# Performance work log

Hardware: AMD Instinct MI355X
Metric: run time of the kernel (lower is better)

Reference implementation:

```python
import jax, jax.numpy as jnp
import numpy as np

D_MODEL = 1024
NUM_HEADS = 16
HEAD_DIM = D_MODEL // NUM_HEADS


def setup_inputs() -> dict:
    key = jax.random.key(0)
    ks = jax.random.split(key, 9)
    B, L, D = 2, 2048, D_MODEL
    s = 1.0 / np.sqrt(D)
    return {
        "x": jax.random.normal(ks[0], (B, L, D), dtype=jnp.float32),
        "Wq": jax.random.normal(ks[1], (D, D), dtype=jnp.float32) * s,
        "bq": jax.random.normal(ks[2], (D,), dtype=jnp.float32) * 0.01,
        "Wk": jax.random.normal(ks[3], (D, D), dtype=jnp.float32) * s,
        "bk": jax.random.normal(ks[4], (D,), dtype=jnp.float32) * 0.01,
        "Wv": jax.random.normal(ks[5], (D, D), dtype=jnp.float32) * s,
        "bv": jax.random.normal(ks[6], (D,), dtype=jnp.float32) * 0.01,
        "Wo": jax.random.normal(ks[7], (D, D), dtype=jnp.float32) * s,
        "bo": jax.random.normal(ks[8], (D,), dtype=jnp.float32) * 0.01,
    }


def reference(x, Wq, bq, Wk, bk, Wv, bv, Wo, bo):
    B, L, D = x.shape
    H, hd = NUM_HEADS, HEAD_DIM
    # projections (torch Linear: x @ W^T + b)
    q = (x @ Wq.T + bq).reshape(B, L, H, hd).transpose(0, 2, 1, 3)  # [B,H,L,hd]
    k = (x @ Wk.T + bk).reshape(B, L, H, hd).transpose(0, 2, 1, 3)
    v = (x @ Wv.T + bv).reshape(B, L, H, hd).transpose(0, 2, 1, 3)
    scores = jnp.einsum("bhqd,bhkd->bhqk", q, k) / jnp.sqrt(jnp.float32(hd))
    attn = jax.nn.softmax(scores, axis=-1)
    ctx = jnp.einsum("bhqk,bhkd->bhqd", attn, v)  # [B,H,L,hd]
    ctx = ctx.transpose(0, 2, 1, 3).reshape(B, L, D)
    return ctx @ Wo.T + bo
```

## Files before the change

### kernel.cpp

```cpp
#include <hip/hip_runtime.h>
#include <hip/hip_bf16.h>
#include <stdint.h>

typedef __attribute__((ext_vector_type(8))) short short8;
typedef __attribute__((ext_vector_type(4))) float f32x4;
typedef __attribute__((ext_vector_type(16))) float f32x16;
typedef __attribute__((ext_vector_type(4))) unsigned int uint4v;
typedef __attribute__((ext_vector_type(2))) unsigned int uint2v;

#define MFMA16(a, b, c) __builtin_amdgcn_mfma_f32_16x16x32_bf16((a), (b), (c), 0, 0, 0)
#define MFMA32(a, b, c) __builtin_amdgcn_mfma_f32_32x32x16_bf16((a), (b), (c), 0, 0, 0)

#define GLDS16(ldsptr, gptr)                                                                     \
    __builtin_amdgcn_global_load_lds(                                                            \
        (const __attribute__((address_space(1))) unsigned int*)(gptr),                           \
        (__attribute__((address_space(3))) unsigned int*)(ldsptr), 16, 0, 0)

#define WAITCNT(n) asm volatile("s_waitcnt vmcnt(" #n ")" ::: "memory")

__device__ __forceinline__ unsigned short f2bf(float f) {
    union { float f; unsigned u; } v; v.f = f;
    return (unsigned short)((v.u + 0x7FFFu + ((v.u >> 16) & 1u)) >> 16);
}

__device__ __forceinline__ unsigned cvt_pk_bf16(float lo, float hi) {
    unsigned r;
    asm("v_cvt_pk_bf16_f32 %0, %1, %2" : "=v"(r) : "v"(lo), "v"(hi));
    return r;
}

__global__ void cvt_all(const float* __restrict__ x,
                        const float* __restrict__ wq, const float* __restrict__ wk,
                        const float* __restrict__ wv, const float* __restrict__ wo,
                        unsigned short* __restrict__ xb,
                        unsigned short* __restrict__ wqb, unsigned short* __restrict__ wkb,
                        unsigned short* __restrict__ wvb, unsigned short* __restrict__ wob) {
    int bid = blockIdx.x;
    const float* s; unsigned short* d; int off;
    if (bid < 4096) {
        s = x; d = xb; off = bid;
    } else {
        int w = (bid - 4096) >> 10;
        off = (bid - 4096) & 1023;
        switch (w) {
            case 0: s = wq; d = wqb; break;
            case 1: s = wk; d = wkb; break;
            case 2: s = wv; d = wvb; break;
            default: s = wo; d = wob; break;
        }
    }
    int i = off * 256 + threadIdx.x;
    float4 v = reinterpret_cast<const float4*>(s)[i];
    ushort4 o;
    o.x = f2bf(v.x); o.y = f2bf(v.y); o.z = f2bf(v.z); o.w = f2bf(v.w);
    reinterpret_cast<ushort4*>(d)[i] = o;
}

__device__ __forceinline__ void gemm_core_mfma(
    const unsigned short* __restrict__ A, const unsigned short* __restrict__ W,
    unsigned short* sl, int m0, int n0, f32x4 (&acc)[4][4])
{
    const int tid = threadIdx.x;
    const int lane = tid & 63, wid = tid >> 6;
    const int l15 = lane & 15, grp = lane >> 4;
    const int wm = (wid >> 1) * 64, wn = (wid & 1) * 64;
    const int rs_ = tid >> 3, c8 = tid & 7;

    auto stage = [&](int buf, int kt) {
        unsigned short* As = &sl[buf * 16384];
        unsigned short* Bs = &sl[buf * 16384 + 8192];
#pragma unroll
        for (int q = 0; q < 4; ++q) {
            int r = q * 32 + rs_;
            int sc = (c8 ^ (r & 7)) << 3;
            GLDS16(&As[(q * 256 + tid) * 8], &A[(size_t)(m0 + r) * 1024 + kt + sc]);
        }
#pragma unroll
        for (int q = 0; q < 4; ++q) {
            int r = q * 32 + rs_;
            int sc = (c8 ^ (r & 7)) << 3;
            GLDS16(&Bs[(q * 256 + tid) * 8], &W[(size_t)(n0 + r) * 1024 + kt + sc]);
        }
    };

    stage(0, 0);
    for (int t = 0; t < 16; ++t) {
        if (t < 15) {
            stage((t + 1) & 1, (t + 1) * 64);
            WAITCNT(8);
        } else {
            WAITCNT(0);
        }
        __builtin_amdgcn_s_barrier();
        const unsigned short* As = &sl[(t & 1) * 16384];
        const unsigned short* Bs = &sl[(t & 1) * 16384 + 8192];
#pragma unroll
        for (int ks = 0; ks < 2; ++ks) {
            short8 a[4], b[4];
#pragma unroll
            for (int i = 0; i < 4; ++i) {
                int row = wm + i * 16 + l15;
                a[i] = *reinterpret_cast<const short8*>(
                    &As[row * 64 + ((ks * 32 + grp * 8) ^ ((row & 7) << 3))]);
            }
#pragma unroll
            for (int j = 0; j < 4; ++j) {
                int row = wn + j * 16 + l15;
                b[j] = *reinterpret_cast<const short8*>(
                    &Bs[row * 64 + ((ks * 32 + grp * 8) ^ ((row & 7) << 3))]);
            }
#pragma unroll
            for (int i = 0; i < 4; ++i)
#pragma unroll
                for (int j = 0; j < 4; ++j)
                    acc[i][j] = MFMA16(a[i], b[j], acc[i][j]);
        }
        if (t < 15) __builtin_amdgcn_s_barrier();
    }
}

__global__ __launch_bounds__(256, 2) void gemm_qkv(
    const unsigned short* __restrict__ A,
    const unsigned short* __restrict__ W0, const unsigned short* __restrict__ W1,
    const unsigned short* __restrict__ W2,
    const float* __restrict__ b0, const float* __restrict__ b1, const float* __restrict__ b2,
    unsigned short* __restrict__ o0, unsigned short* __restrict__ o1,
    unsigned short* __restrict__ vt_out)
{
    __shared__ __attribute__((aligned(16))) unsigned short sl[32768];

    int id = blockIdx.x + (blockIdx.y << 3) + (blockIdx.z << 8);
    int lg = (id & 7) * 96 + (id >> 3);
    const int bx = lg & 7, by = (lg >> 3) & 31, bz = lg >> 8;

    const unsigned short* W; const float* bias; float oscale;
    if (bz == 0)      { W = W0; bias = b0; oscale = 0.18033688f; }
    else if (bz == 1) { W = W1; bias = b1; oscale = 1.0f; }
    else              { W = W2; bias = b2; oscale = 1.0f; }

    const f32x4 fz = {0.f, 0.f, 0.f, 0.f};
    f32x4 acc[4][4];
#pragma unroll
    for (int i = 0; i < 4; ++i)
#pragma unroll
        for (int j = 0; j < 4; ++j) acc[i][j] = fz;

    const int m0 = by * 128, n0 = bx * 128;
    gemm_core_mfma(A, W, sl, m0, n0, acc);

    const int tid = threadIdx.x, lane = tid & 63, wid = tid >> 6;
    const int l15 = lane & 15, grp = lane >> 4;
    const int wm = (wid >> 1) * 64, wn = (wid & 1) * 64;
    const int bb = m0 >> 11;

    if (bz < 2) {
        unsigned short* out = (bz == 0) ? o0 : o1;
#pragma unroll
        for (int j = 0; j < 4; ++j) {
            int ncol = n0 + wn + j * 16 + l15;
            float bv_ = bias[ncol];
            int h = ncol >> 6, d = ncol & 63;
#pragma unroll
            for (int i = 0; i < 4; ++i)
#pragma unroll
                for (int r = 0; r < 4; ++r) {
                    int mrow = m0 + wm + i * 16 + grp * 4 + r;
                    int ll = mrow & 2047;
                    out[(((size_t)(bb * 16 + h)) * 2048 + ll) * 64 + d] =
                        f2bf((acc[i][j][r] + bv_) * oscale);
                }
        }
    } else {
        __syncthreads();
#pragma unroll
        for (int j = 0; j < 4; ++j) {
            float bv_ = bias[n0 + wn + j * 16 + l15];
#pragma unroll
            for (int i = 0; i < 4; ++i)
#pragma unroll
                for (int r = 0; r < 4; ++r) {
                    int c = wn + j * 16 + l15;
                    int rr = wm + i * 16 + grp * 4 + r;
                    sl[c * 136 + rr] = f2bf(acc[i][j][r] + bv_);
                }
        }
        __syncthreads();
        const int llb = m0 & 2047;
#pragma unroll 4
        for (int it = 0; it < 32; ++it) {
            int c = wid * 32 + it;
            unsigned v = *reinterpret_cast<const unsigned*>(&sl[c * 136 + lane * 2]);
            int ncol = n0 + c;
            size_t row = ((size_t)(bb * 16 + (ncol >> 6))) * 64 + (ncol & 63);
            *reinterpret_cast<unsigned*>(&vt_out[row * 2048 + llb + lane * 2]) = v;
        }
    }
}

__global__ __launch_bounds__(256, 2) void gemm_out(
    const unsigned short* __restrict__ A, const unsigned short* __restrict__ W,
    const float* __restrict__ bias, float* __restrict__ out)
{
    __shared__ __attribute__((aligned(16))) unsigned short sl[32768];

    int id = blockIdx.x + (blockIdx.y << 3);
    int lg = (id & 7) * 32 + (id >> 3);
    const int bx = lg & 7, by = lg >> 3;

    const f32x4 fz = {0.f, 0.f, 0.f, 0.f};
    f32x4 acc[4][4];
#pragma unroll
    for (int i = 0; i < 4; ++i)
#pragma unroll
        for (int j = 0; j < 4; ++j) acc[i][j] = fz;

    const int m0 = by * 128, n0 = bx * 128;
    gemm_core_mfma(A, W, sl, m0, n0, acc);

    const int tid = threadIdx.x, lane = tid & 63, wid = tid >> 6;
    const int l15 = lane & 15, grp = lane >> 4;
    const int wm = (wid >> 1) * 64, wn = (wid & 1) * 64;
#pragma unroll
    for (int j = 0; j < 4; ++j) {
        int ncol = n0 + wn + j * 16 + l15;
        float bv_ = bias[ncol];
#pragma unroll
        for (int i = 0; i < 4; ++i)
#pragma unroll
            for (int r = 0; r < 4; ++r) {
                int mrow = m0 + wm + i * 16 + grp * 4 + r;
                out[(size_t)mrow * 1024 + ncol] = acc[i][j][r] + bv_;
            }
    }
}

__global__ __launch_bounds__(512, 2) void attn_kernel(
    const unsigned short* __restrict__ Q,
    const unsigned short* __restrict__ Kg,
    const unsigned short* __restrict__ VTg,
    unsigned short* __restrict__ CTX)
{
    __shared__ __attribute__((aligned(16))) unsigned short k_s[4][4096];
    __shared__ __attribute__((aligned(16))) unsigned short vt_s[4][4096];

    const int tid = threadIdx.x, lane = tid & 63, wid = tid >> 6;
    const int l31 = lane & 31, h = lane >> 5;

    int id = blockIdx.x + (blockIdx.y << 3);
    int lg = ((id & 7) << 5) + (id >> 3);
    const int qt = lg & 7, bh = lg >> 3;

    const int rs_ = tid >> 3, c8 = tid & 7;
    const size_t kvbase = (size_t)bh * 2048 * 64;
    const size_t qbase = kvbase + (size_t)qt * 256 * 64;
    const int scv = (c8 ^ (rs_ & 7)) << 3;

    auto stageKV = [&](int t) {
        int b = t & 3;
        GLDS16(&k_s[b][tid * 8], &Kg[kvbase + (size_t)(t * 64 + rs_) * 64 + scv]);
        GLDS16(&vt_s[b][tid * 8], &VTg[kvbase + (size_t)rs_ * 2048 + t * 64 + scv]);
    };

    short8 aq[4];
    {
        const unsigned short* qp = &Q[qbase + (size_t)(wid * 32 + l31) * 64 + h * 8];
#pragma unroll
        for (int kq = 0; kq < 4; ++kq)
            aq[kq] = *reinterpret_cast<const short8*>(qp + kq * 16);
    }
    stageKV(0);
    stageKV(1);

    short8 ones;
#pragma unroll
    for (int i = 0; i < 8; ++i) ones[i] = (short)0x3F80;

    f32x16 acc[2], acc_l;
#pragma unroll
    for (int i = 0; i < 16; ++i) { acc[0][i] = 0.f; acc[1][i] = 0.f; acc_l[i] = 0.f; }

#pragma unroll 4
    for (int t = 0; t < 32; ++t) {
        if (t < 30) {
            stageKV(t + 2);
            WAITCNT(4);
        } else if (t == 30) {
            WAITCNT(2);
        } else {
            WAITCNT(0);
        }
        __builtin_amdgcn_s_barrier();
        const unsigned short* kcur = k_s[t & 3];
        const unsigned short* vcur = vt_s[t & 3];

        f32x16 st[2];
#pragma unroll
        for (int i = 0; i < 16; ++i) { st[0][i] = 0.f; st[1][i] = 0.f; }
#pragma unroll
        for (int kb = 0; kb < 2; ++kb)
#pragma unroll
            for (int kq = 0; kq < 4; ++kq) {
                int row = kb * 32 + l31;
                short8 ak = *reinterpret_cast<const short8*>(
                    &kcur[row * 64 + ((kq * 16 + h * 8) ^ ((row & 7) << 3))]);
                st[kb] = MFMA32(ak, aq[kq], st[kb]);
            }

        unsigned pk[2][4][2];
#pragma unroll
        for (int kb = 0; kb < 2; ++kb)
#pragma unroll
            for (int g = 0; g < 4; ++g)
#pragma unroll
                for (int p = 0; p < 2; ++p)
                    pk[kb][g][p] = cvt_pk_bf16(
                        __builtin_amdgcn_exp2f(st[kb][4 * g + 2 * p]),
                        __builtin_amdgcn_exp2f(st[kb][4 * g + 2 * p + 1]));

        union { uint4v u; short8 s; } ap[4];
#pragma unroll
        for (int kb = 0; kb < 2; ++kb)
#pragma unroll
            for (int j = 0; j < 2; ++j) {
                uint2v s0 = __builtin_amdgcn_permlane32_swap(
                    pk[kb][2 * j][0], pk[kb][2 * j + 1][0], false, false);
                uint2v s1 = __builtin_amdgcn_permlane32_swap(
                    pk[kb][2 * j][1], pk[kb][2 * j + 1][1], false, false);
                ap[2 * kb + j].u = (uint4v){s0[0], s1[0], s0[1], s1[1]};
            }

        __builtin_amdgcn_s_setprio(1);
#pragma unroll
        for (int kk = 0; kk < 4; ++kk) {
            acc_l = MFMA32(ap[kk].s, ones, acc_l);
#pragma unroll
            for (int db = 0; db < 2; ++db) {
                int row = db * 32 + l31;
                short8 bv = *reinterpret_cast<const short8*>(
                    &vcur[row * 64 + ((kk * 16 + h * 8) ^ ((row & 7) << 3))]);
                acc[db] = MFMA32(ap[kk].s, bv, acc[db]);
            }
        }
        __builtin_amdgcn_s_setprio(0);
    }

    const int b = bh >> 4, hh = bh & 15;
#pragma unroll
    for (int r = 0; r < 16; ++r) {
        int q_local = (r & 3) + 8 * (r >> 2) + 4 * h;
        int qrow = qt * 256 + wid * 32 + q_local;
        float inv = 1.0f / acc_l[r];
#pragma unroll
        for (int db = 0; db < 2; ++db)
            CTX[((size_t)(b * 2048 + qrow)) * 1024 + hh * 64 + db * 32 + l31] =
                f2bf(acc[db][r] * inv);
    }
}

extern "C" void kernel_launch(void* const* d_in, const int* in_sizes, int n_in,
                              void* d_out, int out_size, void* d_ws, size_t ws_size,
                              hipStream_t stream) {
    const float* x  = (const float*)d_in[0];
    const float* Wq = (const float*)d_in[1];
    const float* bq = (const float*)d_in[2];
    const float* Wk = (const float*)d_in[3];
    const float* bk = (const float*)d_in[4];
    const float* Wv = (const float*)d_in[5];
    const float* bv = (const float*)d_in[6];
    const float* Wo = (const float*)d_in[7];
    const float* bo = (const float*)d_in[8];
    float* out = (float*)d_out;

    char* ws = (char*)d_ws;
    unsigned short* xb  = (unsigned short*)(ws + ((size_t)0));
    unsigned short* wqb = (unsigned short*)(ws + ((size_t)8  << 20));
    unsigned short* wkb = (unsigned short*)(ws + ((size_t)10 << 20));
    unsigned short* wvb = (unsigned short*)(ws + ((size_t)12 << 20));
    unsigned short* wob = (unsigned short*)(ws + ((size_t)14 << 20));
    unsigned short* qb  = (unsigned short*)(ws + ((size_t)16 << 20));
    unsigned short* kb  = (unsigned short*)(ws + ((size_t)24 << 20));
    unsigned short* vt  = (unsigned short*)(ws + ((size_t)32 << 20));
    unsigned short* ctx = (unsigned short*)(ws + ((size_t)0));

    cvt_all<<<8192, 256, 0, stream>>>(x, Wq, Wk, Wv, Wo, xb, wqb, wkb, wvb, wob);

    gemm_qkv<<<dim3(8, 32, 3), 256, 0, stream>>>(xb, wqb, wkb, wvb, bq, bk, bv, qb, kb, vt);
    attn_kernel<<<dim3(8, 32), 512, 0, stream>>>(qb, kb, vt, ctx);
    gemm_out<<<dim3(8, 32), 256, 0, stream>>>(ctx, wob, bo, out);
}
```

Before: 96.75 us.

## Split attention KV tiles across wave pairs and reduce partials through LDS

Each attention block now covers 128 query rows instead of 256, using 512 blocks instead of 256. Within a block, two wave groups each handle half of every 64-key tile for the same 32 query rows. Their partial context and row-sum accumulators are combined through shared memory at the end, and launch bounds ask for 4 blocks per CU. This raises parallelism and occupancy to hide latency, at the cost of twice the K/V tile loads per query, extra barriers, an LDS reduction, and register pressure from the higher occupancy target.

New measurement: 101.0 us. 4.4% more time.

```diff
diff --git a/kernel.cpp b/kernel.cpp
--- a/kernel.cpp
+++ b/kernel.cpp
@@ -234,7 +234,7 @@
     }
 }
 
-__global__ __launch_bounds__(512, 2) void attn_kernel(
+__global__ __launch_bounds__(512, 4) void attn_kernel(
     const unsigned short* __restrict__ Q,
     const unsigned short* __restrict__ Kg,
     const unsigned short* __restrict__ VTg,
@@ -245,14 +245,15 @@
 
     const int tid = threadIdx.x, lane = tid & 63, wid = tid >> 6;
     const int l31 = lane & 31, h = lane >> 5;
-
-    int id = blockIdx.x + (blockIdx.y << 3);
-    int lg = ((id & 7) << 5) + (id >> 3);
-    const int qt = lg & 7, bh = lg >> 3;
+    const int qg = wid & 3, kh = wid >> 2;
+
+    int id = blockIdx.x + (blockIdx.y << 4);
+    int lg = ((id & 7) << 6) + (id >> 3);
+    const int qt = lg & 15, bh = lg >> 4;
 
     const int rs_ = tid >> 3, c8 = tid & 7;
     const size_t kvbase = (size_t)bh * 2048 * 64;
-    const size_t qbase = kvbase + (size_t)qt * 256 * 64;
+    const size_t qbase = kvbase + (size_t)qt * 128 * 64;
     const int scv = (c8 ^ (rs_ & 7)) << 3;
 
     auto stageKV = [&](int t) {
@@ -263,7 +264,7 @@
 
     short8 aq[4];
     {
-        const unsigned short* qp = &Q[qbase + (size_t)(wid * 32 + l31) * 64 + h * 8];
+        const unsigned short* qp = &Q[qbase + (size_t)(qg * 32 + l31) * 64 + h * 8];
 #pragma unroll
         for (int kq = 0; kq < 4; ++kq)
             aq[kq] = *reinterpret_cast<const short8*>(qp + kq * 16);
@@ -293,67 +294,88 @@
         const unsigned short* kcur = k_s[t & 3];
         const unsigned short* vcur = vt_s[t & 3];
 
-        f32x16 st[2];
-#pragma unroll
-        for (int i = 0; i < 16; ++i) { st[0][i] = 0.f; st[1][i] = 0.f; }
-#pragma unroll
-        for (int kb = 0; kb < 2; ++kb)
-#pragma unroll
-            for (int kq = 0; kq < 4; ++kq) {
-                int row = kb * 32 + l31;
-                short8 ak = *reinterpret_cast<const short8*>(
-                    &kcur[row * 64 + ((kq * 16 + h * 8) ^ ((row & 7) << 3))]);
-                st[kb] = MFMA32(ak, aq[kq], st[kb]);
-            }
-
-        unsigned pk[2][4][2];
-#pragma unroll
-        for (int kb = 0; kb < 2; ++kb)
-#pragma unroll
-            for (int g = 0; g < 4; ++g)
-#pragma unroll
-                for (int p = 0; p < 2; ++p)
-                    pk[kb][g][p] = cvt_pk_bf16(
-                        __builtin_amdgcn_exp2f(st[kb][4 * g + 2 * p]),
-                        __builtin_amdgcn_exp2f(st[kb][4 * g + 2 * p + 1]));
-
-        union { uint4v u; short8 s; } ap[4];
-#pragma unroll
-        for (int kb = 0; kb < 2; ++kb)
-#pragma unroll
-            for (int j = 0; j < 2; ++j) {
-                uint2v s0 = __builtin_amdgcn_permlane32_swap(
-                    pk[kb][2 * j][0], pk[kb][2 * j + 1][0], false, false);
-                uint2v s1 = __builtin_amdgcn_permlane32_swap(
-                    pk[kb][2 * j][1], pk[kb][2 * j + 1][1], false, false);
-                ap[2 * kb + j].u = (uint4v){s0[0], s1[0], s0[1], s1[1]};
-            }
+        f32x16 st;
+#pragma unroll
+        for (int i = 0; i < 16; ++i) st[i] = 0.f;
+#pragma unroll
+        for (int kq = 0; kq < 4; ++kq) {
+            int row = kh * 32 + l31;
+            short8 ak = *reinterpret_cast<const short8*>(
+                &kcur[row * 64 + ((kq * 16 + h * 8) ^ ((row & 7) << 3))]);
+            st = MFMA32(ak, aq[kq], st);
+        }
+
+        unsigned pk[4][2];
+#pragma unroll
+        for (int g = 0; g < 4; ++g)
+#pragma unroll
+            for (int p = 0; p < 2; ++p)
+                pk[g][p] = cvt_pk_bf16(
+                    __builtin_amdgcn_exp2f(st[4 * g + 2 * p]),
+                    __builtin_amdgcn_exp2f(st[4 * g + 2 * p + 1]));
+
+        union { uint4v u; short8 s; } ap[2];
+#pragma unroll
+        for (int j = 0; j < 2; ++j) {
+            uint2v s0 = __builtin_amdgcn_permlane32_swap(
+                pk[2 * j][0], pk[2 * j + 1][0], false, false);
+            uint2v s1 = __builtin_amdgcn_permlane32_swap(
+                pk[2 * j][1], pk[2 * j + 1][1], false, false);
+            ap[j].u = (uint4v){s0[0], s1[0], s0[1], s1[1]};
+        }
 
         __builtin_amdgcn_s_setprio(1);
 #pragma unroll
-        for (int kk = 0; kk < 4; ++kk) {
-            acc_l = MFMA32(ap[kk].s, ones, acc_l);
+        for (int j = 0; j < 2; ++j) {
+            acc_l = MFMA32(ap[j].s, ones, acc_l);
 #pragma unroll
             for (int db = 0; db < 2; ++db) {
                 int row = db * 32 + l31;
+                int col = (kh * 2 + j) * 16 + h * 8;
                 short8 bv = *reinterpret_cast<const short8*>(
-                    &vcur[row * 64 + ((kk * 16 + h * 8) ^ ((row & 7) << 3))]);
-                acc[db] = MFMA32(ap[kk].s, bv, acc[db]);
+                    &vcur[row * 64 + (col ^ ((row & 7) << 3))]);
+                acc[db] = MFMA32(ap[j].s, bv, acc[db]);
             }
         }
         __builtin_amdgcn_s_setprio(0);
     }
 
-    const int b = bh >> 4, hh = bh & 15;
-#pragma unroll
-    for (int r = 0; r < 16; ++r) {
-        int q_local = (r & 3) + 8 * (r >> 2) + 4 * h;
-        int qrow = qt * 256 + wid * 32 + q_local;
-        float inv = 1.0f / acc_l[r];
-#pragma unroll
-        for (int db = 0; db < 2; ++db)
-            CTX[((size_t)(b * 2048 + qrow)) * 1024 + hh * 64 + db * 32 + l31] =
-                f2bf(acc[db][r] * inv);
+    float* red = reinterpret_cast<float*>(&k_s[0][0]);
+    __syncthreads();
+    if (kh == 1) {
+        float* p = &red[((size_t)qg * 64 + lane) * 32];
+#pragma unroll
+        for (int i = 0; i < 16; ++i) { p[i] = acc[0][i]; p[16 + i] = acc[1][i]; }
+    }
+    __syncthreads();
+    if (kh == 0) {
+        const float* p = &red[((size_t)qg * 64 + lane) * 32];
+#pragma unroll
+        for (int i = 0; i < 16; ++i) { acc[0][i] += p[i]; acc[1][i] += p[16 + i]; }
+    }
+    __syncthreads();
+    if (kh == 1) {
+        float* p = &red[((size_t)qg * 64 + lane) * 16];
+#pragma unroll
+        for (int i = 0; i < 16; ++i) p[i] = acc_l[i];
+    }
+    __syncthreads();
+    if (kh == 0) {
+        const float* p = &red[((size_t)qg * 64 + lane) * 16];
+#pragma unroll
+        for (int i = 0; i < 16; ++i) acc_l[i] += p[i];
+
+        const int b = bh >> 4, hh = bh & 15;
+#pragma unroll
+        for (int r = 0; r < 16; ++r) {
+            int q_local = qg * 32 + (r & 3) + 8 * (r >> 2) + 4 * h;
+            int qrow = qt * 128 + q_local;
+            float inv = 1.0f / acc_l[r];
+#pragma unroll
+            for (int db = 0; db < 2; ++db)
+                CTX[((size_t)(b * 2048 + qrow)) * 1024 + hh * 64 + db * 32 + l31] =
+                    f2bf(acc[db][r] * inv);
+        }
     }
 }
 
@@ -385,6 +407,6 @@
     cvt_all<<<8192, 256, 0, stream>>>(x, Wq, Wk, Wv, Wo, xb, wqb, wkb, wvb, wob);
 
     gemm_qkv<<<dim3(8, 32, 3), 256, 0, stream>>>(xb, wqb, wkb, wvb, bq, bk, bv, qb, kb, vt);
-    attn_kernel<<<dim3(8, 32), 512, 0, stream>>>(qb, kb, vt, ctx);
+    attn_kernel<<<dim3(16, 32), 512, 0, stream>>>(qb, kb, vt, ctx);
     gemm_out<<<dim3(8, 32), 256, 0, stream>>>(ctx, wob, bo, out);
 }
```
